# Optimization experiments

Measured on AMD Instinct MI355X. Metric: run time of the kernel, lower is better.

The kernel has to match this reference:

```python
import jax, jax.numpy as jnp
import numpy as np

N = 20000
E = 320000
F_IN = 50
HID = 64          # hidden_channels
HEADS = 8
WIDTH = HID * HEADS  # 512
NUM_CLASSES = 121


def setup_inputs() -> dict:
    key = jax.random.key(0)
    ks = jax.random.split(key, 16)
    def p(k, shape, fan_in):
        return (jax.random.normal(k, shape, dtype=jnp.float32) / np.sqrt(fan_in)).astype(jnp.float32)
    x = jax.random.normal(ks[0], (N, F_IN), dtype=jnp.float32)
    edge_index = jax.random.randint(ks[1], (2, E), 0, N, dtype=jnp.int64)
    return {
        "x": x,
        "edge_index": edge_index,
        # layer 1: 50 -> 64, heads=8, concat
        "W1": p(ks[2], (F_IN, HEADS * HID), F_IN),
        "a1_src": p(ks[3], (HEADS, HID), HID),
        "a1_dst": p(ks[4], (HEADS, HID), HID),
        "b1": jnp.zeros((HEADS * HID,), jnp.float32),
        # layer 2: 512 -> 512, heads=1, concat
        "W2": p(ks[5], (WIDTH, WIDTH), WIDTH),
        "a2_src": p(ks[6], (1, WIDTH), WIDTH),
        "a2_dst": p(ks[7], (1, WIDTH), WIDTH),
        "b2": jnp.zeros((WIDTH,), jnp.float32),
        # layer 3: 512 -> 121, heads=1, concat=False (mean)
        "W3": p(ks[8], (WIDTH, NUM_CLASSES), WIDTH),
        "a3_src": p(ks[9], (1, NUM_CLASSES), NUM_CLASSES),
        "a3_dst": p(ks[10], (1, NUM_CLASSES), NUM_CLASSES),
        "b3": jnp.zeros((NUM_CLASSES,), jnp.float32),
    }


def gat_conv(x, src, dst, W, a_src, a_dst, b, heads, out_ch, concat):
    n = x.shape[0]
    h = (x @ W).reshape(n, heads, out_ch)                 # [N, H, C]
    al_s = jnp.sum(h * a_src, axis=-1)                     # [N, H]
    al_d = jnp.sum(h * a_dst, axis=-1)                     # [N, H]
    e = jax.nn.leaky_relu(al_s[src] + al_d[dst], 0.2)      # [E, H]
    # edge softmax per destination node (stable)
    m = jax.ops.segment_max(e, dst, num_segments=n)        # [N, H]
    m = jnp.where(jnp.isfinite(m), m, 0.0)
    ex = jnp.exp(e - m[dst])
    z = jax.ops.segment_sum(ex, dst, num_segments=n)       # [N, H]
    alpha = ex / (z[dst] + 1e-16)                          # [E, H]
    msg = h[src] * alpha[..., None]                        # [E, H, C]
    out = jax.ops.segment_sum(msg, dst, num_segments=n)    # [N, H, C]
    out = out.reshape(n, heads * out_ch) if concat else out.mean(axis=1)
    return out + b


def reference(x, edge_index, W1, a1_src, a1_dst, b1, W2, a2_src, a2_dst, b2, W3, a3_src, a3_dst, b3):
    n = x.shape[0]
    # PyG GATConv adds self loops by default
    loops = jnp.arange(n, dtype=edge_index.dtype)
    src = jnp.concatenate([edge_index[0], loops])
    dst = jnp.concatenate([edge_index[1], loops])
    # eval mode: dropout is identity
    x1 = gat_conv(x, src, dst, W1, a1_src, a1_dst, b1, HEADS, HID, True)
    h = jax.nn.elu(x1)
    x1 = gat_conv(h, src, dst, W2, a2_src, a2_dst, b2, 1, WIDTH, True)
    h = jax.nn.elu(x1)
    x1 = gat_conv(h, src, dst, W3, a3_src, a3_dst, b3, 1, NUM_CLASSES, False)
    return x1
```

## Files before the change

### kernel.cpp

```cpp
#include <hip/hip_runtime.h>
#include <hip/hip_bf16.h>
#include <hip/hip_fp16.h>

#define NN     20000
#define ERAW   320000
#define ETOT   (ERAW + NN)
#define F_IN   50
#define HID    64
#define HEADS  8
#define WIDTH  512
#define NCLS   121
#define NCLS_P 128

typedef __attribute__((ext_vector_type(8))) __bf16 bf16x8;
typedef __attribute__((ext_vector_type(4))) float floatx4;

__device__ __forceinline__ unsigned short f32_to_bf16_rn(float f) {
  unsigned u = __float_as_uint(f);
  unsigned r = u + 0x7fffu + ((u >> 16) & 1u);
  return (unsigned short)(r >> 16);
}
__device__ __forceinline__ void split_one(float f, unsigned short& h,
                                          unsigned short& l) {
  h = f32_to_bf16_rn(f);
  float fh = __uint_as_float(((unsigned)h) << 16);
  l = f32_to_bf16_rn(f - fh);
}

__device__ __forceinline__ float2 u2f2(unsigned u) {
  __half2 hv = *reinterpret_cast<__half2*>(&u);
  return __half22float2(hv);
}

__device__ __forceinline__ void gll16(const unsigned short* g,
                                      const unsigned short* l) {
  __builtin_amdgcn_global_load_lds(
      (const __attribute__((address_space(1))) unsigned int*)(const void*)g,
      (__attribute__((address_space(3))) unsigned int*)(void*)l, 16, 0, 0);
}

#define PW_BLOCKS 449
__global__ __launch_bounds__(256) void prep_weights(
    const float* __restrict__ W1, const float* __restrict__ W2,
    const float* __restrict__ W3, const float* __restrict__ a1s,
    const float* __restrict__ a1d, unsigned short* __restrict__ w1hHi,
    unsigned short* __restrict__ w1hLo, unsigned short* __restrict__ w2tHi,
    unsigned short* __restrict__ w2tLo, unsigned short* __restrict__ w3tHi,
    unsigned short* __restrict__ w3tLo, float* __restrict__ w1as,
    float* __restrict__ w1ad) {
  __shared__ float t[32][33];
  const int b = blockIdx.x;
  if (b < 320) {
    const float* W;
    unsigned short *thi, *tlo;
    int M, Mp, bx, by;
    const int K = WIDTH;
    if (b < 256) {
      W = W2; thi = w2tHi; tlo = w2tLo; M = WIDTH; Mp = WIDTH;
      bx = b & 15; by = b >> 4;
    } else {
      int bb = b - 256;
      W = W3; thi = w3tHi; tlo = w3tLo; M = NCLS; Mp = NCLS_P;
      bx = bb & 15; by = bb >> 4;
    }
    int k0 = bx * 32, m0 = by * 32;
    int tx = threadIdx.x & 31, ty = threadIdx.x >> 5;
    #pragma unroll
    for (int r = 0; r < 4; ++r) {
      int k = k0 + ty + r * 8, m = m0 + tx;
      float v = 0.f;
      if (k < K && m < M) v = W[(size_t)k * M + m];
      t[ty + r * 8][tx] = v;
    }
    __syncthreads();
    #pragma unroll
    for (int r = 0; r < 4; ++r) {
      int m = m0 + ty + r * 8, k = k0 + tx;
      if (m < Mp && k < K) {
        unsigned short h, l;
        split_one(t[tx][ty + r * 8], h, l);
        thi[(size_t)m * K + k] = h;
        tlo[(size_t)m * K + k] = l;
      }
    }
  } else if (b < 448) {
    int idx = (b - 320) * 256 + threadIdx.x;
    if (idx < HEADS * HID * HID) {
      int hd = idx >> 12, rem = idx & 4095;
      int col = rem >> 6, k = rem & 63;
      float v = (k < F_IN) ? W1[(size_t)k * WIDTH + hd * HID + col] : 0.f;
      unsigned short h, l;
      split_one(v, h, l);
      w1hHi[idx] = h;
      w1hLo[idx] = l;
    }
  } else {
    for (int idx = threadIdx.x; idx < 2 * F_IN * HEADS; idx += 256) {
      int which = idx >= F_IN * HEADS;
      int r = which ? idx - F_IN * HEADS : idx;
      int k = r >> 3, h = r & 7;
      const float* a = which ? a1d : a1s;
      float s = 0.f;
      for (int c = 0; c < HID; ++c)
        s += W1[(size_t)k * WIDTH + h * HID + c] * a[h * HID + c];
      (which ? w1ad : w1as)[r] = s;
    }
  }
}

__global__ __launch_bounds__(256) void gemm_split_db(
    const unsigned short* __restrict__ Ahi, const unsigned short* __restrict__ Alo,
    const unsigned short* __restrict__ Bthi, const unsigned short* __restrict__ Btlo,
    __half* __restrict__ C16, int N, int K, int M, int Mp, int RB, int CB) {
  __shared__ unsigned short lds[32768];

  const int f = blockIdx.x;
  const int xcd = f & 7;
  const int g = f >> 3;
  const int cb = g % CB;
  const int rb = (g / CB) * 8 + xcd;
  if (rb >= RB) return;
  const int r0 = rb * 128, c0 = cb * 128;

  const int tid = threadIdx.x;
  const int wave = tid >> 6, lane = tid & 63;
  const int wr = wave >> 1, wc = wave & 1;
  const int lkg = lane >> 4, lmn = lane & 15;

  const int rquad = lane >> 2, slot = lane & 3;
  const unsigned short* abase =
      (wave == 0) ? Ahi : (wave == 1) ? Alo : (wave == 2) ? Bthi : Btlo;
  const bool isA = wave < 2;
  const unsigned short* gsrc[8];
  int ldsoff[8];
  #pragma unroll
  for (int i = 0; i < 8; ++i) {
    int r = i * 16 + rquad;
    int c = slot ^ ((r >> 1) & 3);
    size_t grow;
    if (isA) {
      int ra = r0 + r;
      if (ra > N - 1) ra = N - 1;
      grow = (size_t)ra;
    } else {
      grow = (size_t)(c0 + r);
    }
    gsrc[i] = abase + grow * K + c * 8;
    ldsoff[i] = wave * 4096 + i * 512;
  }

  int offA[4], offB[4];
  #pragma unroll
  for (int mi = 0; mi < 4; ++mi) {
    int m = wr * 64 + mi * 16 + lmn;
    offA[mi] = m * 32 + (lkg ^ ((m >> 1) & 3)) * 8;
  }
  #pragma unroll
  for (int ni = 0; ni < 4; ++ni) {
    int n = wc * 64 + ni * 16 + lmn;
    offB[ni] = 8192 + n * 32 + (lkg ^ ((n >> 1) & 3)) * 8;
  }

  floatx4 acc[4][4] = {};

  #pragma unroll
  for (int i = 0; i < 8; ++i) gll16(gsrc[i], lds + ldsoff[i]);

  const int nk = K >> 5;
  for (int t = 0; t < nk; ++t) {
    if (t + 1 < nk) {
      const unsigned short* dst = lds + ((t + 1) & 1) * 16384;
      #pragma unroll
      for (int i = 0; i < 8; ++i)
        gll16(gsrc[i] + (t + 1) * 32, dst + ldsoff[i]);
      asm volatile("s_waitcnt vmcnt(8)" ::: "memory");
    } else {
      asm volatile("s_waitcnt vmcnt(0)" ::: "memory");
    }
    __builtin_amdgcn_sched_barrier(0);
    __builtin_amdgcn_s_barrier();
    __builtin_amdgcn_sched_barrier(0);

    const unsigned short* Lb = lds + (t & 1) * 16384;
    bf16x8 fAhi[4], fAlo[4], fBhi[4], fBlo[4];
    #pragma unroll
    for (int mi = 0; mi < 4; ++mi) {
      fAhi[mi] = *(const bf16x8*)(Lb + offA[mi]);
      fAlo[mi] = *(const bf16x8*)(Lb + 4096 + offA[mi]);
    }
    #pragma unroll
    for (int ni = 0; ni < 4; ++ni) {
      fBhi[ni] = *(const bf16x8*)(Lb + offB[ni]);
      fBlo[ni] = *(const bf16x8*)(Lb + 4096 + offB[ni]);
    }
    #pragma unroll
    for (int mi = 0; mi < 4; ++mi)
      #pragma unroll
      for (int ni = 0; ni < 4; ++ni) {
        acc[mi][ni] = __builtin_amdgcn_mfma_f32_16x16x32_bf16(
            fAhi[mi], fBhi[ni], acc[mi][ni], 0, 0, 0);
        acc[mi][ni] = __builtin_amdgcn_mfma_f32_16x16x32_bf16(
            fAhi[mi], fBlo[ni], acc[mi][ni], 0, 0, 0);
        acc[mi][ni] = __builtin_amdgcn_mfma_f32_16x16x32_bf16(
            fAlo[mi], fBhi[ni], acc[mi][ni], 0, 0, 0);
      }

    __builtin_amdgcn_sched_barrier(0);
    asm volatile("s_waitcnt lgkmcnt(0)" ::: "memory");
    __builtin_amdgcn_s_barrier();
    __builtin_amdgcn_sched_barrier(0);
  }

  #pragma unroll
  for (int mi = 0; mi < 4; ++mi) {
    #pragma unroll
    for (int r = 0; r < 4; ++r) {
      int grow = r0 + wr * 64 + mi * 16 + (lane >> 4) * 4 + r;
      if (grow >= N) continue;
      #pragma unroll
      for (int ni = 0; ni < 4; ++ni) {
        int gcol = c0 + wc * 64 + ni * 16 + lmn;
        float v = (gcol < M) ? acc[mi][ni][r] : 0.f;
        C16[(size_t)grow * Mp + gcol] = __float2half(v);
      }
    }
  }
}

__global__ __launch_bounds__(256) void gemm_l1_heads(
    const unsigned short* __restrict__ Ahi, const unsigned short* __restrict__ Alo,
    const unsigned short* __restrict__ Bthi, const unsigned short* __restrict__ Btlo,
    unsigned short* __restrict__ outHi, unsigned short* __restrict__ outLo,
    const float* __restrict__ bias) {
  __shared__ unsigned short sAhi[8192], sAlo[8192], sBhi[4096], sBlo[4096];
  const int tid = threadIdx.x;
  const int wave = tid >> 6, lane = tid & 63;
  const int r0 = blockIdx.x * 128;
  const int hd = blockIdx.y;
  const int lkg = lane >> 4, lmn = lane & 15;

  #pragma unroll
  for (int t = 0; t < 4; ++t) {
    int cid = tid + t * 256;
    int row = cid >> 3, c = cid & 7;
    int gr = r0 + row; if (gr > NN - 1) gr = NN - 1;
    const size_t goff = (size_t)gr * WIDTH + hd * HID + c * 8;
    int loff = (((c >> 2) * 4 + (c & 3)) * 128 + row) * 8;
    *(uint4*)(sAhi + loff) = *(const uint4*)(Ahi + goff);
    *(uint4*)(sAlo + loff) = *(const uint4*)(Alo + goff);
  }
  #pragma unroll
  for (int t = 0; t < 2; ++t) {
    int cid = tid + t * 256;
    int col = cid >> 3, c = cid & 7;
    const size_t goff = (size_t)(hd * HID + col) * HID + c * 8;
    int loff = (((c >> 2) * 4 + (c & 3)) * 64 + col) * 8;
    *(uint4*)(sBhi + loff) = *(const uint4*)(Bthi + goff);
    *(uint4*)(sBlo + loff) = *(const uint4*)(Btlo + goff);
  }
  __syncthreads();

  floatx4 acc[2][4] = {};
  #pragma unroll
  for (int ks = 0; ks < 2; ++ks) {
    bf16x8 fAhi[2], fAlo[2], fBhi[4], fBlo[4];
    #pragma unroll
    for (int mi = 0; mi < 2; ++mi) {
      int m = wave * 32 + mi * 16 + lmn;
      int off = ((ks * 4 + lkg) * 128 + m) * 8;
      fAhi[mi] = *(const bf16x8*)(sAhi + off);
      fAlo[mi] = *(const bf16x8*)(sAlo + off);
    }
    #pragma unroll
    for (int ni = 0; ni < 4; ++ni) {
      int n = ni * 16 + lmn;
      int off = ((ks * 4 + lkg) * 64 + n) * 8;
      fBhi[ni] = *(const bf16x8*)(sBhi + off);
      fBlo[ni] = *(const bf16x8*)(sBlo + off);
    }
    #pragma unroll
    for (int mi = 0; mi < 2; ++mi)
      #pragma unroll
      for (int ni = 0; ni < 4; ++ni) {
        acc[mi][ni] = __builtin_amdgcn_mfma_f32_16x16x32_bf16(
            fAhi[mi], fBhi[ni], acc[mi][ni], 0, 0, 0);
        acc[mi][ni] = __builtin_amdgcn_mfma_f32_16x16x32_bf16(
            fAhi[mi], fBlo[ni], acc[mi][ni], 0, 0, 0);
        acc[mi][ni] = __builtin_amdgcn_mfma_f32_16x16x32_bf16(
            fAlo[mi], fBhi[ni], acc[mi][ni], 0, 0, 0);
      }
  }

  #pragma unroll
  for (int mi = 0; mi < 2; ++mi) {
    #pragma unroll
    for (int r = 0; r < 4; ++r) {
      int grow = r0 + wave * 32 + mi * 16 + (lane >> 4) * 4 + r;
      if (grow >= NN) continue;
      #pragma unroll
      for (int ni = 0; ni < 4; ++ni) {
        int gcol = hd * HID + ni * 16 + lmn;
        float v = acc[mi][ni][r] + bias[gcol];
        v = (v > 0.f) ? v : (__expf(v) - 1.0f);
        unsigned short hh, ll;
        split_one(v, hh, ll);
        outHi[(size_t)grow * WIDTH + gcol] = hh;
        outLo[(size_t)grow * WIDTH + gcol] = ll;
      }
    }
  }
}

__global__ __launch_bounds__(256) void al1_kernel(
    const float* __restrict__ x, const float* __restrict__ w1as,
    const float* __restrict__ w1ad, float* __restrict__ al_s,
    float* __restrict__ al_d) {
  int n = (blockIdx.x * blockDim.x + threadIdx.x) >> 6;
  int lane = threadIdx.x & 63;
  if (n >= NN) return;
  float xv = (lane < F_IN) ? x[(size_t)n * F_IN + lane] : 0.f;
  float ws[HEADS], wd[HEADS];
  #pragma unroll
  for (int h = 0; h < HEADS; ++h) {
    ws[h] = (lane < F_IN) ? w1as[lane * HEADS + h] : 0.f;
    wd[h] = (lane < F_IN) ? w1ad[lane * HEADS + h] : 0.f;
  }
  #pragma unroll
  for (int h = 0; h < HEADS; ++h) {
    float ss = xv * ws[h], sd = xv * wd[h];
    #pragma unroll
    for (int o = 32; o; o >>= 1) {
      ss += __shfl_xor(ss, o);
      sd += __shfl_xor(sd, o);
    }
    if (lane == 0) {
      al_s[n * HEADS + h] = ss;
      al_d[n * HEADS + h] = sd;
    }
  }
}

template <int C, int CS>
__global__ __launch_bounds__(256) void compute_al16(
    const __half* __restrict__ h16, const float* __restrict__ a_src,
    const float* __restrict__ a_dst, float* __restrict__ al_s,
    float* __restrict__ al_d) {
  int n = (blockIdx.x * blockDim.x + threadIdx.x) >> 6;
  int lane = threadIdx.x & 63;
  if (n >= NN) return;
  const __half* hr = h16 + (size_t)n * CS;
  float ss = 0.f, sd = 0.f;
  if (C % 512 == 0) {
    uint4 raw = *(const uint4*)(hr + lane * 8);
    float f[8];
    float2 t;
    t = u2f2(raw.x); f[0] = t.x; f[1] = t.y;
    t = u2f2(raw.y); f[2] = t.x; f[3] = t.y;
    t = u2f2(raw.z); f[4] = t.x; f[5] = t.y;
    t = u2f2(raw.w); f[6] = t.x; f[7] = t.y;
    #pragma unroll
    for (int j = 0; j < 8; ++j) {
      int c = lane * 8 + j;
      ss += f[j] * a_src[c];
      sd += f[j] * a_dst[c];
    }
  } else {
    for (int c = lane; c < C; c += 64) {
      float v = __half2float(hr[c]);
      ss += v * a_src[c];
      sd += v * a_dst[c];
    }
  }
  #pragma unroll
  for (int o = 32; o; o >>= 1) {
    ss += __shfl_xor(ss, o);
    sd += __shfl_xor(sd, o);
  }
  if (lane == 0) {
    al_s[n] = ss;
    al_d[n] = sd;
  }
}

__global__ __launch_bounds__(256) void count_deg(
    const int* __restrict__ edst, int* __restrict__ deg) {
  int e = blockIdx.x * blockDim.x + threadIdx.x;
  if (e >= ETOT) return;
  int d = (e < ERAW) ? edst[e] : (e - ERAW);
  atomicAdd(&deg[d], 1);
}

__global__ __launch_bounds__(256) void scan_deg(
    const int* __restrict__ deg, int* __restrict__ rowptr) {
  __shared__ int part[256];
  const int t = threadIdx.x;
  const int CHUNK = (NN + 255) / 256;
  int lo = t * CHUNK, hi = min(lo + CHUNK, NN);
  int s = 0;
  for (int i = lo; i < hi; ++i) s += deg[i];
  part[t] = s;
  __syncthreads();
  for (int off = 1; off < 256; off <<= 1) {
    int v = (t >= off) ? part[t - off] : 0;
    __syncthreads();
    part[t] += v;
    __syncthreads();
  }
  int base = (t == 0) ? 0 : part[t - 1];
  for (int i = lo; i < hi; ++i) {
    rowptr[i] = base;
    base += deg[i];
  }
  if (t == 255) rowptr[NN] = part[255];
}

__global__ __launch_bounds__(256) void scatter_csr(
    const int* __restrict__ esrc, const int* __restrict__ edst,
    const int* __restrict__ rowptr, int* __restrict__ cnt,
    int* __restrict__ csrc) {
  int e = blockIdx.x * blockDim.x + threadIdx.x;
  if (e >= ETOT) return;
  int s, d;
  if (e < ERAW) { s = esrc[e]; d = edst[e]; }
  else          { s = e - ERAW; d = e - ERAW; }
  int pos = rowptr[d] + atomicAdd(&cnt[d], 1);
  csrc[pos] = s;
}

__global__ __launch_bounds__(256) void agg_x_sm(
    const int* __restrict__ rowptr, const int* __restrict__ csrc,
    const float* __restrict__ al_s, const float* __restrict__ al_d,
    const float* __restrict__ x, unsigned short* __restrict__ outHi,
    unsigned short* __restrict__ outLo) {
  const int w = threadIdx.x >> 6, lane = threadIdx.x & 63;
  const int d = blockIdx.x * 4 + w;
  if (d >= NN) return;
  const int r0 = rowptr[d], r1 = rowptr[d + 1];
  const int mh = lane & 7;
  const float ald_my = al_d[d * HEADS + mh];
  float m_my = al_s[d * HEADS + mh] + ald_my;
  m_my = (m_my > 0.f) ? m_my : 0.2f * m_my;

  float z_my = 0.f;
  float acc[HEADS];
  #pragma unroll
  for (int hh = 0; hh < HEADS; ++hh) acc[hh] = 0.f;
  for (int p = r0; p < r1; ++p) {
    int s = csrc[p];
    float v = al_s[s * HEADS + mh] + ald_my;
    v = (v > 0.f) ? v : 0.2f * v;
    float a = __expf(v - m_my);
    z_my += a;
    float xv = (lane < F_IN) ? x[(size_t)s * F_IN + lane] : 0.f;
    #pragma unroll
    for (int hh = 0; hh < HEADS; ++hh) acc[hh] += __shfl(a, hh, 8) * xv;
  }
  #pragma unroll
  for (int hh = 0; hh < HEADS; ++hh) {
    float zh = __shfl(z_my, hh, 8);
    float v = (lane < F_IN) ? acc[hh] / (zh + 1e-16f) : 0.f;
    unsigned short h2, l2;
    split_one(v, h2, l2);
    outHi[(size_t)d * WIDTH + hh * HID + lane] = h2;
    outLo[(size_t)d * WIDTH + hh * HID + lane] = l2;
  }
}

template <int M, int MS, bool ELU, bool SPLIT>
__global__ __launch_bounds__(256) void pull_agg_sm(
    const int* __restrict__ rowptr, const int* __restrict__ csrc,
    const float* __restrict__ al_s, const float* __restrict__ al_d,
    const __half* __restrict__ h16, const float* __restrict__ bias,
    float* __restrict__ out, unsigned short* __restrict__ outHi,
    unsigned short* __restrict__ outLo) {
  constexpr int EPL = MS / 64;
  const int w = threadIdx.x >> 6;
  const int lane = threadIdx.x & 63;
  const int d = blockIdx.x * 4 + w;
  if (d >= NN) return;
  const int r0 = rowptr[d], r1 = rowptr[d + 1];
  const float ald = al_d[d];
  float m = al_s[d] + ald;
  m = (m > 0.f) ? m : 0.2f * m;

  const int base = lane * EPL;
  float acc[EPL];
  #pragma unroll
  for (int j = 0; j < EPL; ++j) acc[j] = 0.f;
  float z = 0.f;

  for (int p = r0; p < r1; ++p) {
    int s = csrc[p];
    float v = al_s[s] + ald;
    v = (v > 0.f) ? v : 0.2f * v;
    float a = __expf(v - m);
    z += a;
    const __half* hr = h16 + (size_t)s * MS + base;
    if (EPL == 8) {
      uint4 raw = *(const uint4*)hr;
      float2 f0 = u2f2(raw.x), f1 = u2f2(raw.y);
      float2 f2 = u2f2(raw.z), f3 = u2f2(raw.w);
      acc[0] += f0.x * a; acc[1] += f0.y * a;
      acc[2] += f1.x * a; acc[3] += f1.y * a;
      acc[4] += f2.x * a; acc[5] += f2.y * a;
      acc[6] += f3.x * a; acc[7] += f3.y * a;
    } else if (EPL == 2) {
      unsigned raw = *(const unsigned*)hr;
      float2 f0 = u2f2(raw);
      acc[0] += f0.x * a;
      acc[1] += f0.y * a;
    } else {
      #pragma unroll
      for (int j = 0; j < EPL; ++j) acc[j] += __half2float(hr[j]) * a;
    }
  }
  const float iz = 1.0f / (z + 1e-16f);

  #pragma unroll
  for (int j = 0; j < EPL; ++j) {
    if ((M == MS) || (base + j < M)) {
      float v = acc[j] * iz + bias[base + j];
      if (ELU) v = (v > 0.f) ? v : (__expf(v) - 1.0f);
      if (SPLIT) {
        unsigned short hh, ll;
        split_one(v, hh, ll);
        outHi[(size_t)d * M + base + j] = hh;
        outLo[(size_t)d * M + base + j] = ll;
      } else {
        out[(size_t)d * M + base + j] = v;
      }
    }
  }
}

extern "C" void kernel_launch(void* const* d_in, const int* in_sizes, int n_in,
                              void* d_out, int out_size, void* d_ws,
                              size_t ws_size, hipStream_t stream) {
  const float* x      = (const float*)d_in[0];
  const int*   ei     = (const int*)d_in[1];
  const float* W1     = (const float*)d_in[2];
  const float* a1_src = (const float*)d_in[3];
  const float* a1_dst = (const float*)d_in[4];
  const float* b1     = (const float*)d_in[5];
  const float* W2     = (const float*)d_in[6];
  const float* a2_src = (const float*)d_in[7];
  const float* a2_dst = (const float*)d_in[8];
  const float* b2     = (const float*)d_in[9];
  const float* W3     = (const float*)d_in[10];
  const float* a3_src = (const float*)d_in[11];
  const float* a3_dst = (const float*)d_in[12];
  const float* b3     = (const float*)d_in[13];
  float* out = (float*)d_out;

  const int* esrc = ei;
  const int* edst = ei + ERAW;

  unsigned short* p1Hi  = (unsigned short*)d_ws;
  unsigned short* p1Lo  = p1Hi + (size_t)NN * WIDTH;
  unsigned short* p2Hi  = p1Lo + (size_t)NN * WIDTH;
  unsigned short* p2Lo  = p2Hi + (size_t)NN * WIDTH;
  __half*        h16    = (__half*)(p2Lo + (size_t)NN * WIDTH);
  unsigned short* w1hHi = (unsigned short*)(h16 + (size_t)NN * WIDTH);
  unsigned short* w1hLo = w1hHi + (size_t)HEADS * HID * HID;
  unsigned short* w2tHi = w1hLo + (size_t)HEADS * HID * HID;
  unsigned short* w2tLo = w2tHi + (size_t)WIDTH * WIDTH;
  unsigned short* w3tHi = w2tLo + (size_t)WIDTH * WIDTH;
  unsigned short* w3tLo = w3tHi + (size_t)NCLS_P * WIDTH;
  float* al_s   = (float*)(w3tLo + (size_t)NCLS_P * WIDTH);
  float* al_d   = al_s + (size_t)NN * HEADS;
  float* w1as   = al_d + (size_t)NN * HEADS;
  float* w1ad   = w1as + F_IN * HEADS;
  int* deg      = (int*)(w1ad + F_IN * HEADS);
  int* cnt      = deg + NN;
  int* rowptr   = cnt + NN;
  int* csrc     = rowptr + NN + 4;

  hipMemsetAsync(deg, 0, (size_t)(2 * NN) * sizeof(int), stream);
  const int eblk = (ETOT + 255) / 256;
  count_deg<<<eblk, 256, 0, stream>>>(edst, deg);
  scan_deg<<<1, 256, 0, stream>>>(deg, rowptr);
  scatter_csr<<<eblk, 256, 0, stream>>>(esrc, edst, rowptr, cnt, csrc);

  prep_weights<<<PW_BLOCKS, 256, 0, stream>>>(
      W1, W2, W3, a1_src, a1_dst, w1hHi, w1hLo, w2tHi, w2tLo, w3tHi, w3tLo,
      w1as, w1ad);

  const int nwblk = (NN + 3) / 4;

  al1_kernel<<<nwblk, 256, 0, stream>>>(x, w1as, w1ad, al_s, al_d);
  agg_x_sm<<<nwblk, 256, 0, stream>>>(rowptr, csrc, al_s, al_d, x, p1Hi,
                                      p1Lo);
  gemm_l1_heads<<<dim3((NN + 127) / 128, HEADS), 256, 0, stream>>>(
      p1Hi, p1Lo, w1hHi, w1hLo, p2Hi, p2Lo, b1);

  const int RB = (NN + 127) / 128;
  const int RBG = (RB + 7) / 8;

  gemm_split_db<<<RBG * 8 * (WIDTH / 128), 256, 0, stream>>>(
      p2Hi, p2Lo, w2tHi, w2tLo, h16, NN, WIDTH, WIDTH, WIDTH, RB, WIDTH / 128);
  compute_al16<WIDTH, WIDTH><<<nwblk, 256, 0, stream>>>(h16, a2_src, a2_dst,
                                                        al_s, al_d);
  pull_agg_sm<WIDTH, WIDTH, true, true><<<nwblk, 256, 0, stream>>>(
      rowptr, csrc, al_s, al_d, h16, b2, nullptr, p1Hi, p1Lo);

  gemm_split_db<<<RBG * 8 * (NCLS_P / 128), 256, 0, stream>>>(
      p1Hi, p1Lo, w3tHi, w3tLo, h16, NN, WIDTH, NCLS, NCLS_P, RB,
      NCLS_P / 128);
  compute_al16<NCLS, NCLS_P><<<nwblk, 256, 0, stream>>>(h16, a3_src, a3_dst,
                                                        al_s, al_d);
  pull_agg_sm<NCLS, NCLS_P, false, false><<<nwblk, 256, 0, stream>>>(
      rowptr, csrc, al_s, al_d, h16, b3, out, nullptr, nullptr);
}
```

Measured before the change: 423.0 us.

## Precompute edge softmax weights and split aggregation into 64-column slices

Adds an edge_alpha kernel that computes the per-edge exponentiated attention weights and each node's inverse normaliser once, storing them in workspace. The aggregation becomes pull_agg_slice: each wavefront handles one 64-column slice of one destination node and reads one half per lane per edge, instead of one wavefront per node covering all columns with 8-wide vector loads. This multiplies the grid size for more parallelism and lowers register use, but each edge's csrc and alpha are now re-read once per slice. Per-lane h loads become 2-byte instead of 16-byte, and an extra kernel launch plus edge-array traffic are added.

```diff
diff --git a/kernel.cpp b/kernel.cpp
--- a/kernel.cpp
+++ b/kernel.cpp
@@ -466,69 +466,73 @@
   }
 }
 
-template <int M, int MS, bool ELU, bool SPLIT>
-__global__ __launch_bounds__(256) void pull_agg_sm(
+__global__ __launch_bounds__(256) void edge_alpha(
     const int* __restrict__ rowptr, const int* __restrict__ csrc,
     const float* __restrict__ al_s, const float* __restrict__ al_d,
-    const __half* __restrict__ h16, const float* __restrict__ bias,
-    float* __restrict__ out, unsigned short* __restrict__ outHi,
-    unsigned short* __restrict__ outLo) {
-  constexpr int EPL = MS / 64;
-  const int w = threadIdx.x >> 6;
-  const int lane = threadIdx.x & 63;
+    float* __restrict__ alphaE, float* __restrict__ izv) {
+  const int w = threadIdx.x >> 6, lane = threadIdx.x & 63;
   const int d = blockIdx.x * 4 + w;
   if (d >= NN) return;
   const int r0 = rowptr[d], r1 = rowptr[d + 1];
   const float ald = al_d[d];
   float m = al_s[d] + ald;
   m = (m > 0.f) ? m : 0.2f * m;
-
-  const int base = lane * EPL;
-  float acc[EPL];
-  #pragma unroll
-  for (int j = 0; j < EPL; ++j) acc[j] = 0.f;
   float z = 0.f;
-
-  for (int p = r0; p < r1; ++p) {
-    int s = csrc[p];
-    float v = al_s[s] + ald;
-    v = (v > 0.f) ? v : 0.2f * v;
-    float a = __expf(v - m);
-    z += a;
-    const __half* hr = h16 + (size_t)s * MS + base;
-    if (EPL == 8) {
-      uint4 raw = *(const uint4*)hr;
-      float2 f0 = u2f2(raw.x), f1 = u2f2(raw.y);
-      float2 f2 = u2f2(raw.z), f3 = u2f2(raw.w);
-      acc[0] += f0.x * a; acc[1] += f0.y * a;
-      acc[2] += f1.x * a; acc[3] += f1.y * a;
-      acc[4] += f2.x * a; acc[5] += f2.y * a;
-      acc[6] += f3.x * a; acc[7] += f3.y * a;
-    } else if (EPL == 2) {
-      unsigned raw = *(const unsigned*)hr;
-      float2 f0 = u2f2(raw);
-      acc[0] += f0.x * a;
-      acc[1] += f0.y * a;
+  for (int base = r0; base < r1; base += 64) {
+    int p = base + lane;
+    float a = 0.f;
+    if (p < r1) {
+      int s = csrc[p];
+      float v = al_s[s] + ald;
+      v = (v > 0.f) ? v : 0.2f * v;
+      a = __expf(v - m);
+      alphaE[p] = a;
+    }
+    int cnt = r1 - base; if (cnt > 64) cnt = 64;
+    for (int j = 0; j < cnt; ++j) z += __shfl(a, j);
+  }
+  if (lane == 0) izv[d] = 1.0f / (z + 1e-16f);
+}
+
+template <int MS, int M, bool ELU, bool SPLIT>
+__global__ __launch_bounds__(256) void pull_agg_slice(
+    const int* __restrict__ rowptr, const int* __restrict__ csrc,
+    const float* __restrict__ alphaE, const float* __restrict__ izv,
+    const __half* __restrict__ h16, const float* __restrict__ bias,
+    float* __restrict__ out, unsigned short* __restrict__ outHi,
+    unsigned short* __restrict__ outLo) {
+  constexpr int NSL = MS / 64;
+  const int f = blockIdx.x;
+  const int slice = f % NSL;
+  const int nb = f / NSL;
+  const int w = threadIdx.x >> 6, lane = threadIdx.x & 63;
+  const int d = nb * 4 + w;
+  if (d >= NN) return;
+  const int col = slice * 64 + lane;
+  const int r0 = rowptr[d], r1 = rowptr[d + 1];
+  const __half* hc = h16 + col;
+  float acc = 0.f;
+
+  int p = r0;
+  int s = csrc[p];
+  float a = alphaE[p];
+  for (; p < r1; ++p) {
+    int sn = 0; float an = 0.f;
+    if (p + 1 < r1) { sn = csrc[p + 1]; an = alphaE[p + 1]; }
+    acc += __half2float(hc[(size_t)s * MS]) * a;
+    s = sn; a = an;
+  }
+
+  if (col < M) {
+    float v = acc * izv[d] + bias[col];
+    if (ELU) v = (v > 0.f) ? v : (__expf(v) - 1.0f);
+    if (SPLIT) {
+      unsigned short hh, ll;
+      split_one(v, hh, ll);
+      outHi[(size_t)d * M + col] = hh;
+      outLo[(size_t)d * M + col] = ll;
     } else {
-      #pragma unroll
-      for (int j = 0; j < EPL; ++j) acc[j] += __half2float(hr[j]) * a;
-    }
-  }
-  const float iz = 1.0f / (z + 1e-16f);
-
-  #pragma unroll
-  for (int j = 0; j < EPL; ++j) {
-    if ((M == MS) || (base + j < M)) {
-      float v = acc[j] * iz + bias[base + j];
-      if (ELU) v = (v > 0.f) ? v : (__expf(v) - 1.0f);
-      if (SPLIT) {
-        unsigned short hh, ll;
-        split_one(v, hh, ll);
-        outHi[(size_t)d * M + base + j] = hh;
-        outLo[(size_t)d * M + base + j] = ll;
-      } else {
-        out[(size_t)d * M + base + j] = v;
-      }
+      out[(size_t)d * M + col] = v;
     }
   }
 }
@@ -574,6 +578,8 @@
   int* cnt      = deg + NN;
   int* rowptr   = cnt + NN;
   int* csrc     = rowptr + NN + 4;
+  float* alphaE = (float*)(csrc + ETOT);
+  float* izv    = alphaE + ETOT;
 
   hipMemsetAsync(deg, 0, (size_t)(2 * NN) * sizeof(int), stream);
   const int eblk = (ETOT + 255) / 256;
@@ -600,14 +606,18 @@
       p2Hi, p2Lo, w2tHi, w2tLo, h16, NN, WIDTH, WIDTH, WIDTH, RB, WIDTH / 128);
   compute_al16<WIDTH, WIDTH><<<nwblk, 256, 0, stream>>>(h16, a2_src, a2_dst,
                                                         al_s, al_d);
-  pull_agg_sm<WIDTH, WIDTH, true, true><<<nwblk, 256, 0, stream>>>(
-      rowptr, csrc, al_s, al_d, h16, b2, nullptr, p1Hi, p1Lo);
+  edge_alpha<<<nwblk, 256, 0, stream>>>(rowptr, csrc, al_s, al_d, alphaE,
+                                        izv);
+  pull_agg_slice<WIDTH, WIDTH, true, true><<<nwblk * 8, 256, 0, stream>>>(
+      rowptr, csrc, alphaE, izv, h16, b2, nullptr, p1Hi, p1Lo);
 
   gemm_split_db<<<RBG * 8 * (NCLS_P / 128), 256, 0, stream>>>(
       p1Hi, p1Lo, w3tHi, w3tLo, h16, NN, WIDTH, NCLS, NCLS_P, RB,
       NCLS_P / 128);
   compute_al16<NCLS, NCLS_P><<<nwblk, 256, 0, stream>>>(h16, a3_src, a3_dst,
                                                         al_s, al_d);
-  pull_agg_sm<NCLS, NCLS_P, false, false><<<nwblk, 256, 0, stream>>>(
-      rowptr, csrc, al_s, al_d, h16, b3, out, nullptr, nullptr);
-}
+  edge_alpha<<<nwblk, 256, 0, stream>>>(rowptr, csrc, al_s, al_d, alphaE,
+                                        izv);
+  pull_agg_slice<NCLS_P, NCLS, false, false><<<nwblk * 2, 256, 0, stream>>>(
+      rowptr, csrc, alphaE, izv, h16, b3, out, nullptr, nullptr);
+}
```

New measurement: 564.9 us. 1.34x slower.
